# Performance work log

Measured on AMD Instinct MI355X. Metric: run time of the kernel, lower is better.

## Reference

```python
import jax, jax.numpy as jnp
import numpy as np
from jax import lax

B_, CIN, COUT, H, W = 8, 64, 64, 64, 64
DIN, DSTATE, K, DTRANK = 128, 16, 4, 4  # d_inner=2*C, d_state=16, 4 scan dirs, dt_rank=ceil(64/16)


def setup_inputs():
    key = jax.random.key(0)
    ks = jax.random.split(key, 10)
    f = lambda k, s, sc=0.02: jax.random.normal(k, s, jnp.float32) * sc
    return {
        "x": jax.random.normal(ks[0], (B_, CIN, H, W), jnp.float32),
        "conv_w": f(ks[1], (COUT, CIN, 3, 3)),
        "conv_b": jnp.zeros((COUT,), jnp.float32),
        "gn_g": jnp.ones((COUT,), jnp.float32),
        "gn_b": jnp.zeros((COUT,), jnp.float32),
        "ln1_g": jnp.ones((COUT,), jnp.float32),
        "ln1_b": jnp.zeros((COUT,), jnp.float32),
        "in_proj_w": f(ks[2], (COUT, 2 * DIN)),
        "dw_w": f(ks[3], (DIN, 1, 3, 3)),
        "dw_b": jnp.zeros((DIN,), jnp.float32),
        "x_proj_w": f(ks[4], (K, DTRANK + 2 * DSTATE, DIN)),
        "dt_w": f(ks[5], (K, DIN, DTRANK)),
        "dt_b": f(ks[6], (K, DIN), 0.01),
        "A_logs": jnp.tile(jnp.log(jnp.arange(1, DSTATE + 1, dtype=jnp.float32)), (K, DIN, 1)),
        "Ds": jnp.ones((K, DIN), jnp.float32),
        "out_norm_g": jnp.ones((DIN,), jnp.float32),
        "out_norm_b": jnp.zeros((DIN,), jnp.float32),
        "out_proj_w": f(ks[7], (DIN, COUT)),
    }


def _ln(x, g, b, eps=1e-5):
    m = x.mean(-1, keepdims=True)
    v = ((x - m) ** 2).mean(-1, keepdims=True)
    return (x - m) * lax.rsqrt(v + eps) * g + b


def reference(x, conv_w, conv_b, gn_g, gn_b, ln1_g, ln1_b, in_proj_w, dw_w, dw_b,
              x_proj_w, dt_w, dt_b, A_logs, Ds, out_norm_g, out_norm_b, out_proj_w):
    # BasicConv2d: conv3x3 (stride 1, pad 1) + GroupNorm(2) + SiLU
    y = lax.conv_general_dilated(x, conv_w, (1, 1), [(1, 1), (1, 1)],
                                 dimension_numbers=("NCHW", "OIHW", "NCHW"))
    y = y + conv_b[None, :, None, None]
    Bb, C, Hh, Ww = y.shape
    yg = y.reshape(Bb, 2, C // 2, Hh, Ww)
    m = yg.mean((2, 3, 4), keepdims=True)
    v = ((yg - m) ** 2).mean((2, 3, 4), keepdims=True)
    y = ((yg - m) * lax.rsqrt(v + 1e-5)).reshape(Bb, C, Hh, Ww)
    y = y * gn_g[None, :, None, None] + gn_b[None, :, None, None]
    y = jax.nn.silu(y)
    # VSSBlock on NHWC: LN -> SS2D -> residual
    xb = y.transpose(0, 2, 3, 1)                       # (B,H,W,C)
    h = _ln(xb, ln1_g, ln1_b)
    xz = h @ in_proj_w                                 # (B,H,W,2*DIN)
    xm, z = jnp.split(xz, 2, axis=-1)
    xm = xm.transpose(0, 3, 1, 2)                      # (B,DIN,H,W)
    xm = lax.conv_general_dilated(xm, dw_w, (1, 1), [(1, 1), (1, 1)],
                                  dimension_numbers=("NCHW", "OIHW", "NCHW"),
                                  feature_group_count=DIN)
    xm = jax.nn.silu(xm + dw_b[None, :, None, None])
    L = Hh * Ww
    x1 = xm.reshape(Bb, DIN, L)                        # HW order
    x2 = xm.transpose(0, 1, 3, 2).reshape(Bb, DIN, L)  # WH order
    xs = jnp.stack([x1, x2], 1)
    xs = jnp.concatenate([xs, jnp.flip(xs, -1)], 1)    # (B,4,DIN,L)
    xdbl = jnp.einsum("bkdl,kcd->bkcl", xs, x_proj_w)
    dts, Bs, Cs = jnp.split(xdbl, [DTRANK, DTRANK + DSTATE], axis=2)
    dts = jnp.einsum("bkrl,kdr->bkdl", dts, dt_w)
    dt = jax.nn.softplus(dts + dt_b[None, :, :, None])  # (B,4,DIN,L)
    A = -jnp.exp(A_logs)                                # (K,DIN,DSTATE)
    # selective scan over L (time-major)
    u_t = xs.transpose(3, 0, 1, 2)
    dt_t = dt.transpose(3, 0, 1, 2)
    B_t = Bs.transpose(3, 0, 1, 2)
    C_t = Cs.transpose(3, 0, 1, 2)

    def step(hst, inp):
        u, d, Bc, Cc = inp
        hst = hst * jnp.exp(d[..., None] * A) + (d * u)[..., None] * Bc[:, :, None, :]
        return hst, jnp.einsum("bkdn,bkn->bkd", hst, Cc)

    h0 = jnp.zeros((Bb, K, DIN, DSTATE), xs.dtype)
    _, ys = lax.scan(step, h0, (u_t, dt_t, B_t, C_t))  # ys: (L,B,4,DIN)
    out_y = ys.transpose(1, 2, 3, 0) + Ds[None, :, :, None] * xs
    inv_y = jnp.flip(out_y[:, 2:4], -1)
    wh_y = out_y[:, 1].reshape(Bb, DIN, Ww, Hh).transpose(0, 1, 3, 2).reshape(Bb, DIN, L)
    invwh_y = inv_y[:, 1].reshape(Bb, DIN, Ww, Hh).transpose(0, 1, 3, 2).reshape(Bb, DIN, L)
    yv = out_y[:, 0] + inv_y[:, 0] + wh_y + invwh_y    # (B,DIN,L)
    yv = yv.transpose(0, 2, 1).reshape(Bb, Hh, Ww, DIN)
    yv = _ln(yv, out_norm_g, out_norm_b)
    yv = yv * jax.nn.silu(z)
    vss = xb + yv @ out_proj_w                          # VSSBlock residual
    return vss.transpose(0, 3, 1, 2) + y                # MambaDU residual
```

## Files before the change

kernel.cpp:

```cpp
#include <hip/hip_runtime.h>
#include <hip/hip_bf16.h>

#define BD   8
#define CD   64
#define HD   64
#define WD   64
#define LD   4096
#define DINN 128
#define KDIR 4
#define NST  16
#define L2E  1.442695040888963f

typedef const float* fp;

__device__ __forceinline__ float sigm(float x) { return 1.f / (1.f + __expf(-x)); }
__device__ __forceinline__ float softplusf(float x) {
    float e = __expf(-fabsf(x));
    return fmaxf(x, 0.f) + __logf(1.f + e);
}
__device__ __forceinline__ int pmap(int k, int l) {
    int m = (k & 2) ? (LD - 1 - l) : l;
    return (k & 1) ? (((m & 63) << 6) | (m >> 6)) : m;
}

__global__ __launch_bounds__(256) void k_wt(fp cw, float* wt) {
    int id = blockIdx.x * 256 + threadIdx.x;
    if (id >= 64 * 64 * 9) return;
    int co = id & 63; int ciq = id >> 6; int ci = ciq / 9; int q = ciq % 9;
    wt[id] = cw[(co * 64 + ci) * 9 + q];
}

__global__ __launch_bounds__(256, 4) void k_conv(fp x, const float* wt, fp cb,
                                                 float* out0, float* out1) {
    __shared__ float xt[32][3][68];
    int bx = blockIdx.x;
    int half = bx & 1; int bh = bx >> 1; int h = bh & 63; int b = bh >> 6;
    int t = threadIdx.x;
    int ci0 = half << 5;
#pragma unroll
    for (int r = 0; r < 3; r++) {
        int hs = h + r - 1;
        bool ok = (hs >= 0 && hs < 64);
        const float* xrow = x + (((size_t)b * 64 + ci0) * 64 + (ok ? hs : 0)) * 64;
        for (int s = t; s < 2048; s += 256) {
            int ci = s >> 6, w = s & 63;
            xt[ci][r][w + 1] = ok ? xrow[ci * 4096 + w] : 0.f;
        }
    }
    for (int s = t; s < 96; s += 256) {
        int ci = s / 3, r = s - ci * 3;
        xt[ci][r][0] = 0.f; xt[ci][r][65] = 0.f; xt[ci][r][66] = 0.f; xt[ci][r][67] = 0.f;
    }
    __syncthreads();
    int coq = t & 15, wq = t >> 4;
    float acc[4][4];
#pragma unroll
    for (int c = 0; c < 4; c++)
#pragma unroll
        for (int j = 0; j < 4; j++) acc[c][j] = 0.f;

    const float* wbase = wt + (size_t)ci0 * 9 * 64 + coq * 4;
    for (int ci = 0; ci < 32; ci++) {
        float4 wv[9];
#pragma unroll
        for (int q = 0; q < 9; q++) wv[q] = *(const float4*)&wbase[(ci * 9 + q) * 64];
#pragma unroll
        for (int r = 0; r < 3; r++) {
            const float* row = &xt[ci][r][wq * 4];
            float4 f0 = ((const float4*)row)[0], f1 = ((const float4*)row)[1];
            float xr[8] = {f0.x, f0.y, f0.z, f0.w, f1.x, f1.y, f1.z, f1.w};
            float4 wa = wv[r * 3 + 0], wb = wv[r * 3 + 1], wc = wv[r * 3 + 2];
#pragma unroll
            for (int j = 0; j < 4; j++) {
                acc[0][j] += wa.x * xr[j] + wb.x * xr[j + 1] + wc.x * xr[j + 2];
                acc[1][j] += wa.y * xr[j] + wb.y * xr[j + 1] + wc.y * xr[j + 2];
                acc[2][j] += wa.z * xr[j] + wb.z * xr[j + 1] + wc.z * xr[j + 2];
                acc[3][j] += wa.w * xr[j] + wb.w * xr[j + 1] + wc.w * xr[j + 2];
            }
        }
    }
    float* dst = half ? out1 : out0;
#pragma unroll
    for (int cc = 0; cc < 4; cc++) {
        int co = coq * 4 + cc;
        float bias = half ? 0.f : cb[co];
        float4 o;
        o.x = acc[cc][0] + bias; o.y = acc[cc][1] + bias;
        o.z = acc[cc][2] + bias; o.w = acc[cc][3] + bias;
        *(float4*)&dst[((b * 64 + co) * 64 + h) * 64 + wq * 4] = o;
    }
}

__global__ __launch_bounds__(256) void k_gnstats2(const float* c0, const float* c1, float* gstats) {
    int bx = blockIdx.x;
    int slice = bx & 31; int bg = bx >> 5; int g = bg & 1; int b = bg >> 1;
    int t = threadIdx.x;
    size_t base = ((size_t)(b * 64 + g * 32 + slice)) * 4096;
    const float4* p0 = (const float4*)(c0 + base);
    const float4* p1 = (const float4*)(c1 + base);
    float s = 0.f, s2 = 0.f;
#pragma unroll
    for (int i = 0; i < 4; i++) {
        float4 a = p0[t + i * 256], bv = p1[t + i * 256];
        float vx = a.x + bv.x, vy = a.y + bv.y, vz = a.z + bv.z, vw = a.w + bv.w;
        s += vx + vy + vz + vw;
        s2 += vx * vx + vy * vy + vz * vz + vw * vw;
    }
#pragma unroll
    for (int off = 32; off; off >>= 1) { s += __shfl_xor(s, off); s2 += __shfl_xor(s2, off); }
    __shared__ float rs[4], rq[4];
    int wid = t >> 6;
    if ((t & 63) == 0) { rs[wid] = s; rq[wid] = s2; }
    __syncthreads();
    if (t == 0) {
        atomicAdd(&gstats[b * 4 + g * 2 + 0], rs[0] + rs[1] + rs[2] + rs[3]);
        atomicAdd(&gstats[b * 4 + g * 2 + 1], rq[0] + rq[1] + rq[2] + rq[3]);
    }
}

__global__ __launch_bounds__(256) void k_gnapply(const float* c0, const float* c1, const float* gstats,
                                                 fp gng, fp gnb, float* y_nhwc) {
    __shared__ float tile[64][65];
    int bx = blockIdx.x; int b = bx >> 6; int p0 = (bx & 63) * 64;
    int t = threadIdx.x;
    const float invN = 1.f / (32.f * 4096.f);
    float s0 = gstats[b * 4 + 0], q0 = gstats[b * 4 + 1];
    float s1 = gstats[b * 4 + 2], q1 = gstats[b * 4 + 3];
    float m0 = s0 * invN, r0 = rsqrtf(q0 * invN - m0 * m0 + 1e-5f);
    float m1 = s1 * invN, r1 = rsqrtf(q1 * invN - m1 * m1 + 1e-5f);
    for (int idx = t; idx < 4096; idx += 256) {
        int c = idx >> 6, pi = idx & 63;
        size_t gi = (size_t)(b * 64 + c) * LD + p0 + pi;
        float v = c0[gi] + c1[gi];
        float mean = (c < 32) ? m0 : m1, rstd = (c < 32) ? r0 : r1;
        v = (v - mean) * rstd * gng[c] + gnb[c];
        v = v * sigm(v);
        tile[c][pi] = v;
    }
    __syncthreads();
    for (int idx = t; idx < 4096; idx += 256) {
        int pi = idx >> 6, c = idx & 63;
        y_nhwc[(b * LD + p0 + pi) * 64 + c] = tile[c][pi];
    }
}

__global__ __launch_bounds__(256) void k_lninproj(const float* y_nhwc, fp lng, fp lnb, fp ipw,
                                                  float* xmc, float* zsil) {
    __shared__ float hn[4][64];
    int bp0 = blockIdx.x * 4;
    int t = threadIdx.x;
    int pix = t >> 6, lane = t & 63;
    {
        float v = y_nhwc[(bp0 + pix) * 64 + lane];
        float s = v, s2 = v * v;
#pragma unroll
        for (int off = 32; off; off >>= 1) { s += __shfl_xor(s, off); s2 += __shfl_xor(s2, off); }
        float mean = s * (1.f / 64.f);
        float rstd = rsqrtf(s2 * (1.f / 64.f) - mean * mean + 1e-5f);
        hn[pix][lane] = (v - mean) * rstd * lng[lane] + lnb[lane];
    }
    __syncthreads();
    float a0 = 0.f, a1 = 0.f, a2 = 0.f, a3 = 0.f;
    for (int c = 0; c < 64; c++) {
        float w = ipw[c * 256 + t];
        a0 += hn[0][c] * w; a1 += hn[1][c] * w; a2 += hn[2][c] * w; a3 += hn[3][c] * w;
    }
    float accv[4] = {a0, a1, a2, a3};
#pragma unroll
    for (int p = 0; p < 4; p++) {
        int bp = bp0 + p;
        float v = accv[p];
        if (t < 128) xmc[bp * 128 + t] = v;
        else         zsil[bp * 128 + (t - 128)] = v * sigm(v);
    }
}

__global__ __launch_bounds__(256) void k_dwconv(const float* xmc, fp dww, fp dwb, float* xm_dw) {
    int id = blockIdx.x * 256 + threadIdx.x;
    int d = id & 127, p = (id >> 7) & (LD - 1), b = id >> 19;
    int h = p >> 6, w = p & 63;
    float wv[9];
#pragma unroll
    for (int q = 0; q < 9; q++) wv[q] = dww[d * 9 + q];
    float acc = dwb[d];
#pragma unroll
    for (int i = 0; i < 3; i++) {
        int hs = h + i - 1; if (hs < 0 || hs > 63) continue;
#pragma unroll
        for (int j = 0; j < 3; j++) {
            int ws = w + j - 1; if (ws < 0 || ws > 63) continue;
            acc += xmc[((b << 12) + (hs << 6) + ws) * 128 + d] * wv[i * 3 + j];
        }
    }
    acc = acc * sigm(acc);
    xm_dw[id] = acc;
}

__global__ __launch_bounds__(192) void k_proj(const float* xm_dw, fp xpw, float* dts4, float* xBC) {
    __shared__ float u_lds[128 * 65];
    int bx = blockIdx.x;
    int lt = bx & 63; int bk = bx >> 6; int k = bk & 3; int b = bk >> 2;
    int l0 = lt * 64;
    int t = threadIdx.x;
    for (int idx = t; idx < 64 * 128; idx += 192) {
        int l = idx >> 7, d = idx & 127;
        u_lds[d * 65 + l] = xm_dw[(b * LD + pmap(k, l0 + l)) * 128 + d];
    }
    __syncthreads();
    int l = t & 63;
    int cgu = __builtin_amdgcn_readfirstlane(t >> 6);
    const float* wg = xpw + (size_t)(k * 36 + cgu * 12) * 128;
    float acc[12];
#pragma unroll
    for (int i = 0; i < 12; i++) acc[i] = 0.f;
    for (int d = 0; d < 128; d += 4) {
        float u0 = u_lds[(d + 0) * 65 + l];
        float u1 = u_lds[(d + 1) * 65 + l];
        float u2 = u_lds[(d + 2) * 65 + l];
        float u3 = u_lds[(d + 3) * 65 + l];
#pragma unroll
        for (int i = 0; i < 12; i++) {
            float4 wv = *(const float4*)&wg[i * 128 + d];
            acc[i] += wv.x * u0 + wv.y * u1 + wv.z * u2 + wv.w * u3;
        }
    }
    int base = bk * LD + l0 + l;
#pragma unroll
    for (int i = 0; i < 12; i++) {
        int c = cgu * 12 + i;
        if (c < 4) dts4[base * 4 + c] = acc[i];
        else       xBC[base * 32 + (c - 4)] = acc[i];
    }
}

__global__ __launch_bounds__(128) void k_scan1(const float* xm_dw, const float* dts4, const float* xBC,
                                               fp dtw, fp dtbp, fp alog,
                                               float* Pbuf, float* Hbuf, int NCr, int CLr) {
    __shared__ float s_b[64 * 16];
    __shared__ float s_d4[64 * 4];
    int c = blockIdx.x, k = blockIdx.y, b = blockIdx.z;
    int d = threadIdx.x;
    int bk = b * 4 + k;
    int kd = k * 128 + d;
    float w0 = dtw[kd * 4 + 0], w1 = dtw[kd * 4 + 1], w2 = dtw[kd * 4 + 2], w3 = dtw[kd * 4 + 3];
    float dtb = dtbp[kd];
    float base = -__expf(alog[kd * 16]) * L2E;
    float A2[16];
    bool geo = true;
#pragma unroll
    for (int n = 0; n < 16; n++) {
        A2[n] = -__expf(alog[kd * 16 + n]) * L2E;
        float ideal = (float)(n + 1) * base;
        geo = geo && (fabsf(A2[n] - ideal) <= 1e-4f * fabsf(ideal));
    }
    float h[16]; float sdt = 0.f;
#pragma unroll
    for (int n = 0; n < 16; n++) h[n] = 0.f;
    int l0 = c * CLr;
    for (int ss = 0; ss < CLr; ss += 64) {
        if (ss) __syncthreads();
        int ls = l0 + ss;
        const float4* gd = (const float4*)&dts4[(size_t)(bk * LD + ls) * 4];
        if (d < 64) ((float4*)s_d4)[d] = gd[d];
        const float4* gx = (const float4*)&xBC[(size_t)(bk * LD + ls) * 32];
        for (int i = d; i < 64 * 4; i += 128) { int s = i >> 2, q = i & 3; ((float4*)s_b)[i] = gx[s * 8 + q]; }
        __syncthreads();
        int pbase = pmap(k, ls);
        int pstep = pmap(k, ls + 1) - pbase;
        const float* up = xm_dw + (size_t)(b * LD + pbase) * 128 + d;
        long ustep = (long)pstep * 128;
        if (geo) {
#pragma unroll 4
            for (int s = 0; s < 64; s++) {
                float4 dv = ((const float4*)s_d4)[s];
                float dtv = softplusf(dv.x * w0 + dv.y * w1 + dv.z * w2 + dv.w * w3 + dtb);
                sdt += dtv;
                float u = *up; up += ustep;
                float du = dtv * u;
                const float4* Bp = (const float4*)&s_b[s * 16];
                float4 B0 = Bp[0], B1 = Bp[1], B2 = Bp[2], B3 = Bp[3];
                float r = exp2f(dtv * base);
                float r2 = r * r, r3 = r2 * r, r4 = r2 * r2;
                float r5 = r4 * r, r6 = r4 * r2, r7 = r4 * r3, r8 = r4 * r4;
                float r9 = r8 * r, r10 = r8 * r2, r11 = r8 * r3, r12 = r8 * r4;
                float r13 = r8 * r5, r14 = r8 * r6, r15 = r8 * r7, r16 = r8 * r8;
                h[0]  = r   * h[0]  + du * B0.x;  h[1]  = r2  * h[1]  + du * B0.y;
                h[2]  = r3  * h[2]  + du * B0.z;  h[3]  = r4  * h[3]  + du * B0.w;
                h[4]  = r5  * h[4]  + du * B1.x;  h[5]  = r6  * h[5]  + du * B1.y;
                h[6]  = r7  * h[6]  + du * B1.z;  h[7]  = r8  * h[7]  + du * B1.w;
                h[8]  = r9  * h[8]  + du * B2.x;  h[9]  = r10 * h[9]  + du * B2.y;
                h[10] = r11 * h[10] + du * B2.z;  h[11] = r12 * h[11] + du * B2.w;
                h[12] = r13 * h[12] + du * B3.x;  h[13] = r14 * h[13] + du * B3.y;
                h[14] = r15 * h[14] + du * B3.z;  h[15] = r16 * h[15] + du * B3.w;
            }
        } else {
#pragma unroll 2
            for (int s = 0; s < 64; s++) {
                float4 dv = ((const float4*)s_d4)[s];
                float dtv = softplusf(dv.x * w0 + dv.y * w1 + dv.z * w2 + dv.w * w3 + dtb);
                sdt += dtv;
                float u = *up; up += ustep;
                float du = dtv * u;
                const float* Bp = &s_b[s * 16];
#pragma unroll
                for (int n = 0; n < 16; n++) {
                    float a = exp2f(dtv * A2[n]);
                    h[n] = a * h[n] + du * Bp[n];
                }
            }
        }
    }
    int obase = (bk * NCr + c) * 2048 + d;
#pragma unroll
    for (int n = 0; n < 16; n++) {
        Pbuf[obase + n * 128] = exp2f(sdt * A2[n]);
        Hbuf[obase + n * 128] = h[n];
    }
}

__global__ __launch_bounds__(256) void k_scan2(const float* Pbuf, const float* Hbuf, float* Hinit, int NCr) {
    int id = blockIdx.x * 256 + threadIdx.x;
    int nd = id & 2047; int bk = id >> 11;
    float h = 0.f;
    int base = bk * NCr * 2048 + nd;
    for (int c = 0; c < NCr; c++) {
        int idx = base + c * 2048;
        Hinit[idx] = h;
        h = Hbuf[idx] + Pbuf[idx] * h;
    }
}

__global__ __launch_bounds__(128) void k_scan3(const float* xm_dw, const float* dts4, const float* xBC,
                                               fp dtw, fp dtbp, fp alog, fp dsp,
                                               const float* Hinit, float* yv, int NCr, int CLr) {
    __shared__ float s_bc[64 * 32];
    __shared__ float s_d4[64 * 4];
    int c = blockIdx.x, k = blockIdx.y, b = blockIdx.z;
    int d = threadIdx.x;
    int bk = b * 4 + k;
    int kd = k * 128 + d;
    float w0 = dtw[kd * 4 + 0], w1 = dtw[kd * 4 + 1], w2 = dtw[kd * 4 + 2], w3 = dtw[kd * 4 + 3];
    float dtb = dtbp[kd];
    float Dv = dsp[kd];
    float base = -__expf(alog[kd * 16]) * L2E;
    float A2[16];
    bool geo = true;
#pragma unroll
    for (int n = 0; n < 16; n++) {
        A2[n] = -__expf(alog[kd * 16 + n]) * L2E;
        float ideal = (float)(n + 1) * base;
        geo = geo && (fabsf(A2[n] - ideal) <= 1e-4f * fabsf(ideal));
    }
    int hbase = (bk * NCr + c) * 2048 + d;
    float h[16];
#pragma unroll
    for (int n = 0; n < 16; n++) h[n] = Hinit[hbase + n * 128];
    int l0 = c * CLr;
    for (int ss = 0; ss < CLr; ss += 64) {
        if (ss) __syncthreads();
        int ls = l0 + ss;
        const float4* gd = (const float4*)&dts4[(size_t)(bk * LD + ls) * 4];
        if (d < 64) ((float4*)s_d4)[d] = gd[d];
        const float4* gx = (const float4*)&xBC[(size_t)(bk * LD + ls) * 32];
        for (int i = d; i < 64 * 8; i += 128) ((float4*)s_bc)[i] = gx[i];
        __syncthreads();
        int pbase = pmap(k, ls);
        int pstep = pmap(k, ls + 1) - pbase;
        const float* up = xm_dw + (size_t)(b * LD + pbase) * 128 + d;
        float* yp = yv + (size_t)(b * LD + pbase) * 128 + d;
        long ustep = (long)pstep * 128;
        if (geo) {
#pragma unroll 4
            for (int s = 0; s < 64; s++) {
                float4 dv = ((const float4*)s_d4)[s];
                float dtv = softplusf(dv.x * w0 + dv.y * w1 + dv.z * w2 + dv.w * w3 + dtb);
                float u = *up; up += ustep;
                float du = dtv * u;
                const float4* Bp = (const float4*)&s_bc[s * 32];
                float4 B0 = Bp[0], B1 = Bp[1], B2 = Bp[2], B3 = Bp[3];
                float4 C0 = Bp[4], C1 = Bp[5], C2 = Bp[6], C3 = Bp[7];
                float r = exp2f(dtv * base);
                float r2 = r * r, r3 = r2 * r, r4 = r2 * r2;
                float r5 = r4 * r, r6 = r4 * r2, r7 = r4 * r3, r8 = r4 * r4;
                float r9 = r8 * r, r10 = r8 * r2, r11 = r8 * r3, r12 = r8 * r4;
                float r13 = r8 * r5, r14 = r8 * r6, r15 = r8 * r7, r16 = r8 * r8;
                float y;
                h[0]  = r   * h[0]  + du * B0.x;  y  = h[0]  * C0.x;
                h[1]  = r2  * h[1]  + du * B0.y;  y += h[1]  * C0.y;
                h[2]  = r3  * h[2]  + du * B0.z;  y += h[2]  * C0.z;
                h[3]  = r4  * h[3]  + du * B0.w;  y += h[3]  * C0.w;
                h[4]  = r5  * h[4]  + du * B1.x;  y += h[4]  * C1.x;
                h[5]  = r6  * h[5]  + du * B1.y;  y += h[5]  * C1.y;
                h[6]  = r7  * h[6]  + du * B1.z;  y += h[6]  * C1.z;
                h[7]  = r8  * h[7]  + du * B1.w;  y += h[7]  * C1.w;
                h[8]  = r9  * h[8]  + du * B2.x;  y += h[8]  * C2.x;
                h[9]  = r10 * h[9]  + du * B2.y;  y += h[9]  * C2.y;
                h[10] = r11 * h[10] + du * B2.z;  y += h[10] * C2.z;
                h[11] = r12 * h[11] + du * B2.w;  y += h[11] * C2.w;
                h[12] = r13 * h[12] + du * B3.x;  y += h[12] * C3.x;
                h[13] = r14 * h[13] + du * B3.y;  y += h[13] * C3.y;
                h[14] = r15 * h[14] + du * B3.z;  y += h[14] * C3.z;
                h[15] = r16 * h[15] + du * B3.w;  y += h[15] * C3.w;
                y += Dv * u;
                atomicAdd(yp, y); yp += ustep;
            }
        } else {
#pragma unroll 2
            for (int s = 0; s < 64; s++) {
                float4 dv = ((const float4*)s_d4)[s];
                float dtv = softplusf(dv.x * w0 + dv.y * w1 + dv.z * w2 + dv.w * w3 + dtb);
                float u = *up; up += ustep;
                float du = dtv * u;
                const float* Bp = &s_bc[s * 32];
                float y = 0.f;
#pragma unroll
                for (int n = 0; n < 16; n++) {
                    float a = exp2f(dtv * A2[n]);
                    h[n] = a * h[n] + du * Bp[n];
                    y += h[n] * Bp[16 + n];
                }
                y += Dv * u;
                atomicAdd(yp, y); yp += ustep;
            }
        }
    }
}

__global__ __launch_bounds__(256) void k_final(const float* yv, const float* zsil, const float* y_nhwc,
                                               fp ong, fp onb, fp opw, float* out) {
    __shared__ float ylds[2][128];
    __shared__ float red[2][2][2];
    __shared__ float part[2][2][64];
    int bp0 = blockIdx.x * 2;
    int t = threadIdx.x;
    int pix = t >> 7, tl = t & 127;
    int bp = bp0 + pix;
    float v = yv[bp * 128 + tl];
    float s = v, s2 = v * v;
#pragma unroll
    for (int off = 32; off; off >>= 1) { s += __shfl_xor(s, off); s2 += __shfl_xor(s2, off); }
    int wh = (t >> 6) & 1;
    if ((t & 63) == 0) { red[pix][wh][0] = s; red[pix][wh][1] = s2; }
    __syncthreads();
    float S = red[pix][0][0] + red[pix][1][0], S2 = red[pix][0][1] + red[pix][1][1];
    float mean = S * (1.f / 128.f);
    float rstd = rsqrtf(S2 * (1.f / 128.f) - mean * mean + 1e-5f);
    float vn = (v - mean) * rstd * ong[tl] + onb[tl];
    vn *= zsil[bp * 128 + tl];
    ylds[pix][tl] = vn;
    __syncthreads();
    {
        int px = t >> 7, half = (t >> 6) & 1, co = t & 63;
        float acc = 0.f;
        const float* yrow = &ylds[px][half * 64];
        const float* wcol = &opw[half * 64 * 64 + co];
#pragma unroll 16
        for (int dd = 0; dd < 64; dd++) acc += yrow[dd] * wcol[dd * 64];
        part[px][half][co] = acc;
    }
    __syncthreads();
    if (t < 128) {
        int pp = t >> 6, co = t & 63;
        int bpo = bp0 + pp;
        float a = part[pp][0][co] + part[pp][1][co];
        float yb = y_nhwc[bpo * 64 + co];
        out[((bpo >> 12) * 64 + co) * LD + (bpo & 4095)] = 2.f * yb + a;
    }
}

extern "C" void kernel_launch(void* const* d_in, const int* in_sizes, int n_in,
                              void* d_out, int out_size, void* d_ws, size_t ws_size,
                              hipStream_t stream) {
    fp x    = (fp)d_in[0];
    fp cw   = (fp)d_in[1];
    fp cb   = (fp)d_in[2];
    fp gng  = (fp)d_in[3];
    fp gnb  = (fp)d_in[4];
    fp lng  = (fp)d_in[5];
    fp lnb  = (fp)d_in[6];
    fp ipw  = (fp)d_in[7];
    fp dww  = (fp)d_in[8];
    fp dwb  = (fp)d_in[9];
    fp xpw  = (fp)d_in[10];
    fp dtw  = (fp)d_in[11];
    fp dtb  = (fp)d_in[12];
    fp alog = (fp)d_in[13];
    fp dsp  = (fp)d_in[14];
    fp ong  = (fp)d_in[15];
    fp onb  = (fp)d_in[16];
    fp opw  = (fp)d_in[17];

    float* w = (float*)d_ws;
    float* conv_out0 = w;  w += BD * 64 * LD;
    float* conv_out1 = w;  w += BD * 64 * LD;
    float* y_nhwc    = w;  w += BD * LD * 64;
    float* gstats    = w;  w += 32;
    float* wt        = w;  w += 64 * 64 * 9;
    float* xmc       = w;  w += BD * LD * 128;
    float* zsil      = w;  w += BD * LD * 128;
    float* xm_dw     = w;  w += BD * LD * 128;
    float* dts4      = w;  w += BD * KDIR * LD * 4;
    float* xBC       = w;  w += BD * KDIR * LD * 32;
    float* yv        = w;  w += BD * LD * 128;
    size_t base_floats = (size_t)(w - (float*)d_ws);

    int NCr = 32;
    size_t perbuf64 = (size_t)32 * 64 * 2048;
    float *Pbuf, *Hbuf, *Hinit;
    if (ws_size >= (base_floats + 3 * perbuf64) * sizeof(float)) {
        NCr = 64;
        Pbuf  = w;  w += perbuf64;
        Hbuf  = w;  w += perbuf64;
        Hinit = w;  w += perbuf64;
    } else {
        Pbuf  = xmc;
        Hbuf  = xmc + (size_t)32 * 32 * 2048;
        Hinit = conv_out0;
    }
    int CLr = LD / NCr;
    if (ws_size < base_floats * sizeof(float)) return;

    hipMemsetAsync(gstats, 0, 32 * sizeof(float), stream);
    k_wt<<<144, 256, 0, stream>>>(cw, wt);
    k_conv<<<BD * HD * 2, 256, 0, stream>>>(x, wt, cb, conv_out0, conv_out1);
    k_gnstats2<<<BD * 2 * 32, 256, 0, stream>>>(conv_out0, conv_out1, gstats);
    k_gnapply<<<BD * 64, 256, 0, stream>>>(conv_out0, conv_out1, gstats, gng, gnb, y_nhwc);
    k_lninproj<<<BD * LD / 4, 256, 0, stream>>>(y_nhwc, lng, lnb, ipw, xmc, zsil);
    k_dwconv<<<BD * LD * 128 / 256, 256, 0, stream>>>(xmc, dww, dwb, xm_dw);
    k_proj<<<BD * KDIR * 64, 192, 0, stream>>>(xm_dw, xpw, dts4, xBC);
    k_scan1<<<dim3(NCr, KDIR, BD), 128, 0, stream>>>(xm_dw, dts4, xBC, dtw, dtb, alog, Pbuf, Hbuf, NCr, CLr);
    k_scan2<<<256, 256, 0, stream>>>(Pbuf, Hbuf, Hinit, NCr);
    hipMemsetAsync(yv, 0, (size_t)BD * LD * 128 * sizeof(float), stream);
    k_scan3<<<dim3(NCr, KDIR, BD), 128, 0, stream>>>(xm_dw, dts4, xBC, dtw, dtb, alog, dsp, Hinit, yv, NCr, CLr);
    k_final<<<BD * LD / 2, 256, 0, stream>>>(yv, zsil, y_nhwc, ong, onb, opw, (float*)d_out);
}
```

Baseline: 449.0 us.

## Replace scan output atomics with per-direction buffers and share projection loads

k_scan3 now writes each scan direction's output to its own buffer with plain stores, reusing dead workspace regions (Pbuf, xmc, conv_out0), instead of atomicAdd into one zeroed buffer. k_final sums the four buffers, and the memset is skipped. k_proj also pairs each forward direction with its reversed counterpart, so one block loads the gathered xm_dw tile once and computes both, halving the gather traffic. The cost is four separate output buffers to read in the final kernel, and correctness depends on the reused buffers being dead at that point.

Measured after the change: 424.6 us. -5.5%, faster.

```diff
diff --git a/kernel.cpp b/kernel.cpp
--- a/kernel.cpp
+++ b/kernel.cpp
@@ -196,20 +196,23 @@
     xm_dw[id] = acc;
 }
 
-__global__ __launch_bounds__(192) void k_proj(const float* xm_dw, fp xpw, float* dts4, float* xBC) {
+__global__ __launch_bounds__(384) void k_proj(const float* xm_dw, fp xpw, float* dts4, float* xBC) {
     __shared__ float u_lds[128 * 65];
     int bx = blockIdx.x;
-    int lt = bx & 63; int bk = bx >> 6; int k = bk & 3; int b = bk >> 2;
+    int lt = bx & 63; int bkp = bx >> 6; int kp = bkp & 1; int b = bkp >> 1;
     int l0 = lt * 64;
     int t = threadIdx.x;
-    for (int idx = t; idx < 64 * 128; idx += 192) {
+    for (int idx = t; idx < 64 * 128; idx += 384) {
         int l = idx >> 7, d = idx & 127;
-        u_lds[d * 65 + l] = xm_dw[(b * LD + pmap(k, l0 + l)) * 128 + d];
+        u_lds[d * 65 + l] = xm_dw[(b * LD + pmap(kp, l0 + l)) * 128 + d];
     }
     __syncthreads();
     int l = t & 63;
-    int cgu = __builtin_amdgcn_readfirstlane(t >> 6);
-    const float* wg = xpw + (size_t)(k * 36 + cgu * 12) * 128;
+    int w = t >> 6;
+    int cgu  = __builtin_amdgcn_readfirstlane(w >> 1);
+    int rev  = __builtin_amdgcn_readfirstlane(w & 1);
+    int ksel = rev ? (kp + 2) : kp;
+    const float* wg = xpw + (size_t)(ksel * 36 + cgu * 12) * 128;
     float acc[12];
 #pragma unroll
     for (int i = 0; i < 12; i++) acc[i] = 0.f;
@@ -224,7 +227,8 @@
             acc[i] += wv.x * u0 + wv.y * u1 + wv.z * u2 + wv.w * u3;
         }
     }
-    int base = bk * LD + l0 + l;
+    int pos = rev ? (LD - 1 - l0 - l) : (l0 + l);
+    int base = (b * 4 + ksel) * LD + pos;
 #pragma unroll
     for (int i = 0; i < 12; i++) {
         int c = cgu * 12 + i;
@@ -332,13 +336,16 @@
 
 __global__ __launch_bounds__(128) void k_scan3(const float* xm_dw, const float* dts4, const float* xBC,
                                                fp dtw, fp dtbp, fp alog, fp dsp,
-                                               const float* Hinit, float* yv, int NCr, int CLr) {
+                                               const float* Hinit,
+                                               float* yv0, float* yv1, float* yv2, float* yv3,
+                                               int multi, int NCr, int CLr) {
     __shared__ float s_bc[64 * 32];
     __shared__ float s_d4[64 * 4];
     int c = blockIdx.x, k = blockIdx.y, b = blockIdx.z;
     int d = threadIdx.x;
     int bk = b * 4 + k;
     int kd = k * 128 + d;
+    float* yvb = multi ? ((k == 0) ? yv0 : (k == 1) ? yv1 : (k == 2) ? yv2 : yv3) : yv0;
     float w0 = dtw[kd * 4 + 0], w1 = dtw[kd * 4 + 1], w2 = dtw[kd * 4 + 2], w3 = dtw[kd * 4 + 3];
     float dtb = dtbp[kd];
     float Dv = dsp[kd];
@@ -367,7 +374,7 @@
         int pbase = pmap(k, ls);
         int pstep = pmap(k, ls + 1) - pbase;
         const float* up = xm_dw + (size_t)(b * LD + pbase) * 128 + d;
-        float* yp = yv + (size_t)(b * LD + pbase) * 128 + d;
+        float* yp = yvb + (size_t)(b * LD + pbase) * 128 + d;
         long ustep = (long)pstep * 128;
         if (geo) {
 #pragma unroll 4
@@ -402,7 +409,8 @@
                 h[14] = r15 * h[14] + du * B3.z;  y += h[14] * C3.z;
                 h[15] = r16 * h[15] + du * B3.w;  y += h[15] * C3.w;
                 y += Dv * u;
-                atomicAdd(yp, y); yp += ustep;
+                if (multi) { *yp = y; } else { atomicAdd(yp, y); }
+                yp += ustep;
             }
         } else {
 #pragma unroll 2
@@ -420,13 +428,16 @@
                     y += h[n] * Bp[16 + n];
                 }
                 y += Dv * u;
-                atomicAdd(yp, y); yp += ustep;
+                if (multi) { *yp = y; } else { atomicAdd(yp, y); }
+                yp += ustep;
             }
         }
     }
 }
 
-__global__ __launch_bounds__(256) void k_final(const float* yv, const float* zsil, const float* y_nhwc,
+__global__ __launch_bounds__(256) void k_final(const float* yv0, const float* yv1,
+                                               const float* yv2, const float* yv3, int multi,
+                                               const float* zsil, const float* y_nhwc,
                                                fp ong, fp onb, fp opw, float* out) {
     __shared__ float ylds[2][128];
     __shared__ float red[2][2][2];
@@ -435,7 +446,9 @@
     int t = threadIdx.x;
     int pix = t >> 7, tl = t & 127;
     int bp = bp0 + pix;
-    float v = yv[bp * 128 + tl];
+    size_t gi = (size_t)bp * 128 + tl;
+    float v = yv0[gi];
+    if (multi) v += yv1[gi] + yv2[gi] + yv3[gi];
     float s = v, s2 = v * v;
 #pragma unroll
     for (int off = 32; off; off >>= 1) { s += __shfl_xor(s, off); s2 += __shfl_xor(s2, off); }
@@ -446,7 +459,7 @@
     float mean = S * (1.f / 128.f);
     float rstd = rsqrtf(S2 * (1.f / 128.f) - mean * mean + 1e-5f);
     float vn = (v - mean) * rstd * ong[tl] + onb[tl];
-    vn *= zsil[bp * 128 + tl];
+    vn *= zsil[gi];
     ylds[pix][tl] = vn;
     __syncthreads();
     {
@@ -504,18 +517,22 @@
     float* yv        = w;  w += BD * LD * 128;
     size_t base_floats = (size_t)(w - (float*)d_ws);
 
-    int NCr = 32;
+    int NCr = 32, multi = 0;
     size_t perbuf64 = (size_t)32 * 64 * 2048;
-    float *Pbuf, *Hbuf, *Hinit;
+    float *Pbuf, *Hbuf, *Hinit, *yv1, *yv2, *yv3;
     if (ws_size >= (base_floats + 3 * perbuf64) * sizeof(float)) {
-        NCr = 64;
+        NCr = 64; multi = 1;
         Pbuf  = w;  w += perbuf64;
         Hbuf  = w;  w += perbuf64;
         Hinit = w;  w += perbuf64;
+        yv1 = Pbuf;
+        yv2 = xmc;
+        yv3 = conv_out0;
     } else {
         Pbuf  = xmc;
         Hbuf  = xmc + (size_t)32 * 32 * 2048;
         Hinit = conv_out0;
+        yv1 = yv2 = yv3 = yv;
     }
     int CLr = LD / NCr;
     if (ws_size < base_floats * sizeof(float)) return;
@@ -527,10 +544,11 @@
     k_gnapply<<<BD * 64, 256, 0, stream>>>(conv_out0, conv_out1, gstats, gng, gnb, y_nhwc);
     k_lninproj<<<BD * LD / 4, 256, 0, stream>>>(y_nhwc, lng, lnb, ipw, xmc, zsil);
     k_dwconv<<<BD * LD * 128 / 256, 256, 0, stream>>>(xmc, dww, dwb, xm_dw);
-    k_proj<<<BD * KDIR * 64, 192, 0, stream>>>(xm_dw, xpw, dts4, xBC);
+    k_proj<<<BD * 2 * 64, 384, 0, stream>>>(xm_dw, xpw, dts4, xBC);
     k_scan1<<<dim3(NCr, KDIR, BD), 128, 0, stream>>>(xm_dw, dts4, xBC, dtw, dtb, alog, Pbuf, Hbuf, NCr, CLr);
     k_scan2<<<256, 256, 0, stream>>>(Pbuf, Hbuf, Hinit, NCr);
-    hipMemsetAsync(yv, 0, (size_t)BD * LD * 128 * sizeof(float), stream);
-    k_scan3<<<dim3(NCr, KDIR, BD), 128, 0, stream>>>(xm_dw, dts4, xBC, dtw, dtb, alog, dsp, Hinit, yv, NCr, CLr);
-    k_final<<<BD * LD / 2, 256, 0, stream>>>(yv, zsil, y_nhwc, ong, onb, opw, (float*)d_out);
-}
+    if (!multi) hipMemsetAsync(yv, 0, (size_t)BD * LD * 128 * sizeof(float), stream);
+    k_scan3<<<dim3(NCr, KDIR, BD), 128, 0, stream>>>(xm_dw, dts4, xBC, dtw, dtb, alog, dsp, Hinit,
+                                                     yv, yv1, yv2, yv3, multi, NCr, CLr);
+    k_final<<<BD * LD / 2, 256, 0, stream>>>(yv, yv1, yv2, yv3, multi, zsil, y_nhwc, ong, onb, opw, (float*)d_out);
+}
```
